# Kernel optimization log

Measured on AMD Instinct MI355X. Metric: run time of the kernel, lower is better.

Reference implementation:

```python
import jax, jax.numpy as jnp
import numpy as np

EMBED_DIM = 1024
NUM_HEADS = 16
HEAD_DIM = EMBED_DIM // NUM_HEADS
SCALING = HEAD_DIM ** -0.5


def setup_inputs() -> dict:
    key = jax.random.key(0)
    ks = jax.random.split(key, 9)
    T, B, E = 2048, 4, EMBED_DIM
    s = 0.02
    return {
        "query": jax.random.normal(ks[0], (T, B, E), dtype=jnp.float32),
        "Wq": jax.random.normal(ks[1], (E, E), dtype=jnp.float32) * s,
        "bq": jnp.zeros((E,), dtype=jnp.float32),
        "Wk": jax.random.normal(ks[2], (E, E), dtype=jnp.float32) * s,
        "bk": jnp.zeros((E,), dtype=jnp.float32),
        "Wv": jax.random.normal(ks[3], (E, E), dtype=jnp.float32) * s,
        "bv": jnp.zeros((E,), dtype=jnp.float32),
        "Wo": jax.random.normal(ks[4], (E, E), dtype=jnp.float32) * s,
        "bo": jnp.zeros((E,), dtype=jnp.float32),
    }


def reference(query, Wq, bq, Wk, bk, Wv, bv, Wo, bo):
    # query: [T, B, E]; torch Linear: x @ W.T + b
    T, B, E = query.shape
    H, D = NUM_HEADS, HEAD_DIM
    q = (query @ Wq.T + bq) * SCALING
    k = query @ Wk.T + bk
    v = query @ Wv.T + bv
    # [T, B, E] -> [B*H, T, D]
    def split_heads(x):
        return x.reshape(T, B * H, D).transpose(1, 0, 2)
    q, k, v = split_heads(q), split_heads(k), split_heads(v)
    attn_weights = jnp.einsum("btd,bsd->bts", q, k)  # [B*H, T, T]
    attn_probs = jax.nn.softmax(attn_weights, axis=-1)
    attn = jnp.einsum("bts,bsd->btd", attn_probs, v)  # [B*H, T, D]
    attn = attn.transpose(1, 0, 2).reshape(T, B, E)
    return attn @ Wo.T + bo
```

## Files before the change

### kernel.cpp

```cpp
#include <hip/hip_runtime.h>
#include <stdint.h>

#define TSEQ   2048
#define BATCH  4
#define NHEAD  16
#define HDIM   64
#define EMB    1024
#define MROWS  (TSEQ * BATCH)
#define QKV_N  (3 * EMB)
#define SCALE_Q 0.125f
#define LOG2E  1.4426950408889634f
#define CB2    (3.0f * LOG2E)

typedef __bf16  bf16x8  __attribute__((ext_vector_type(8)));
typedef __bf16  bf16x2  __attribute__((ext_vector_type(2)));
typedef short   s16x8   __attribute__((ext_vector_type(8)));
typedef float   f32x4   __attribute__((ext_vector_type(4)));
typedef float   f32x16  __attribute__((ext_vector_type(16)));

__device__ __forceinline__ uint16_t b16c(float f) {
    __bf16 h = (__bf16)f;
    return __builtin_bit_cast(uint16_t, h);
}
__device__ __forceinline__ uint32_t pk2(float a, float b) {
    bf16x2 h; h[0] = (__bf16)a; h[1] = (__bf16)b;
    return __builtin_bit_cast(uint32_t, h);
}
__device__ __forceinline__ float exp2hw(float x) {
    float r; asm("v_exp_f32 %0, %1" : "=v"(r) : "v"(x)); return r;
}
__device__ __forceinline__ bf16x8 ldfrag(const uint16_t* p) {
    return __builtin_bit_cast(bf16x8, *(const s16x8*)p);
}
__device__ __forceinline__ f32x4 MFMA(bf16x8 a, bf16x8 b, f32x4 c) {
    return __builtin_amdgcn_mfma_f32_16x16x32_bf16(a, b, c, 0, 0, 0);
}
__device__ __forceinline__ f32x16 MFMA32(bf16x8 a, bf16x8 b, f32x16 c) {
    return __builtin_amdgcn_mfma_f32_32x32x16_bf16(a, b, c, 0, 0, 0);
}

#define GLOAD_LDS16(g, l) \
    __builtin_amdgcn_global_load_lds((const __attribute__((address_space(1))) void*)(g), \
                                     (__attribute__((address_space(3))) void*)(l), 16, 0, 0)

__global__ void cvt_f2b4(const float* __restrict__ src, uint16_t* __restrict__ dst, int n4) {
    int i = blockIdx.x * blockDim.x + threadIdx.x;
    if (i >= n4) return;
    float4 v = ((const float4*)src)[i];
    ushort4 o;
    o.x = b16c(v.x); o.y = b16c(v.y); o.z = b16c(v.z); o.w = b16c(v.w);
    ((ushort4*)dst)[i] = o;
}

__global__ void cvt_wqkv(const float* __restrict__ Wq, const float* __restrict__ Wk,
                         const float* __restrict__ Wv, const float* __restrict__ bq,
                         const float* __restrict__ bk, const float* __restrict__ bv,
                         uint16_t* __restrict__ Wqkv, float* __restrict__ bqkv, int n4) {
    int i = blockIdx.x * blockDim.x + threadIdx.x;
    if (i < QKV_N) {
        float bval;
        if (i < EMB)            bval = bq[i] * SCALE_Q;
        else if (i < 2 * EMB)   bval = bk[i - EMB];
        else                    bval = bv[i - 2 * EMB];
        bqkv[i] = bval;
    }
    if (i >= n4) return;
    int e = i * 4;
    int n = e >> 10;
    int k = e & 1023;
    const float* src; float sc;
    if (n < EMB)            { src = Wq + ((size_t)n << 10) + k;             sc = SCALE_Q; }
    else if (n < 2 * EMB)   { src = Wk + ((size_t)(n - EMB) << 10) + k;     sc = 1.f; }
    else                    { src = Wv + ((size_t)(n - 2 * EMB) << 10) + k; sc = 1.f; }
    float4 v = *(const float4*)src;
    ushort4 o;
    o.x = b16c(v.x * sc); o.y = b16c(v.y * sc); o.z = b16c(v.z * sc); o.w = b16c(v.w * sc);
    ((ushort4*)Wqkv)[i] = o;
}

template <typename CT>
__global__ __launch_bounds__(256) void gemm_bt(
        const uint16_t* __restrict__ A, const uint16_t* __restrict__ Bt,
        const float* __restrict__ bias, CT* __restrict__ C,
        int M, int N, int K, int tiles_n) {
    __shared__ uint16_t As[128 * 32];
    __shared__ uint16_t Bs[128 * 32];

    const int nwg = gridDim.x;
    const int bid0 = blockIdx.x;
    const int bid = (bid0 & 7) * (nwg >> 3) + (bid0 >> 3);
    const int tm = bid / tiles_n, tn = bid % tiles_n;
    const int tid = threadIdx.x;
    const int l = tid & 63, w = tid >> 6;
    const int wm = w >> 1, wn = w & 1;
    const int fr = l & 15, fq = l >> 4;

    f32x4 acc[4][4] = {};

    const int row_a = tid >> 2;
    const int kblk  = (tid & 3) << 3;
    const uint16_t* gA0 = A  + (size_t)(tm * 128 + row_a) * K + kblk;
    const uint16_t* gB0 = Bt + (size_t)(tn * 128 + row_a) * K + kblk;
    const uint16_t* gA1 = gA0 + (size_t)64 * K;
    const uint16_t* gB1 = gB0 + (size_t)64 * K;
    uint16_t* lA0 = As + w * 512;
    uint16_t* lA1 = As + 2048 + w * 512;
    uint16_t* lB0 = Bs + w * 512;
    uint16_t* lB1 = Bs + 2048 + w * 512;

    for (int k0 = 0; k0 < K; k0 += 32) {
        GLOAD_LDS16(gA0 + k0, lA0);
        GLOAD_LDS16(gA1 + k0, lA1);
        GLOAD_LDS16(gB0 + k0, lB0);
        GLOAD_LDS16(gB1 + k0, lB1);
        __syncthreads();

        bf16x8 a[4], b[4];
#pragma unroll
        for (int i = 0; i < 4; i++)
            a[i] = ldfrag(&As[(wm * 64 + i * 16 + fr) * 32 + fq * 8]);
#pragma unroll
        for (int i = 0; i < 4; i++)
            b[i] = ldfrag(&Bs[(wn * 64 + i * 16 + fr) * 32 + fq * 8]);
#pragma unroll
        for (int i = 0; i < 4; i++)
#pragma unroll
            for (int j = 0; j < 4; j++)
                acc[i][j] = MFMA(a[i], b[j], acc[i][j]);
        __syncthreads();
    }

#pragma unroll
    for (int j = 0; j < 4; j++) {
        const int col = tn * 128 + wn * 64 + j * 16 + fr;
        const float bv = bias[col];
#pragma unroll
        for (int i = 0; i < 4; i++) {
#pragma unroll
            for (int r = 0; r < 4; r++) {
                const int row = tm * 128 + wm * 64 + i * 16 + fq * 4 + r;
                const float v = acc[i][j][r] + bv;
                if constexpr (sizeof(CT) == 2) C[(size_t)row * N + col] = (CT)b16c(v);
                else                           C[(size_t)row * N + col] = (CT)v;
            }
        }
    }
}

#define SWZK(r) ((((r) & 3) ^ (((r) >> 2) & 3)))

__global__ __launch_bounds__(512, 2) void gemm_qkv(
        const uint16_t* __restrict__ A, const uint16_t* __restrict__ Bt,
        const float* __restrict__ bias, uint16_t* __restrict__ C) {
    __shared__ __align__(16) uint16_t lds[4 * 16384];

    const int bid0 = blockIdx.x;
    const int bid = (bid0 & 7) * 48 + (bid0 >> 3);
    const int tm = bid / 12, tn = bid % 12;
    const int tid = threadIdx.x;
    const int w = tid >> 6, l = tid & 63;
    const int wm = w >> 2, wn = w & 3;
    const int l5 = l & 31, hi = l >> 5;

    const uint16_t* gA[2]; const uint16_t* gB[2];
    int ldsA[2], ldsB[2];
#pragma unroll
    for (int i = 0; i < 2; i++) {
        int c = i * 512 + tid;
        int row = c >> 2, fqp = c & 3;
        gA[i] = A  + (size_t)(tm * 256 + row) * 1024 + ((fqp ^ SWZK(row)) * 8);
        gB[i] = Bt + (size_t)(tn * 256 + row) * 1024 + ((fqp ^ SWZK(row)) * 8);
        ldsA[i] = (i * 512 + w * 64) * 8;
        ldsB[i] = 8192 + (i * 512 + w * 64) * 8;
    }

    int aoff[4][2], boff[2][2];
#pragma unroll
    for (int mf = 0; mf < 4; mf++) {
        int row = wm * 128 + mf * 32 + l5;
#pragma unroll
        for (int ks = 0; ks < 2; ks++)
            aoff[mf][ks] = row * 32 + (((ks * 2 + hi) ^ SWZK(row)) * 8);
    }
#pragma unroll
    for (int nf = 0; nf < 2; nf++) {
        int row = wn * 64 + nf * 32 + l5;
#pragma unroll
        for (int ks = 0; ks < 2; ks++)
            boff[nf][ks] = 8192 + row * 32 + (((ks * 2 + hi) ^ SWZK(row)) * 8);
    }

    f32x16 acc[4][2] = {};

#define STAGE_T(t, s)                                            \
    {                                                            \
        uint16_t* base_ = lds + (s) * 16384;                     \
        GLOAD_LDS16(gA[0] + (t) * 32, base_ + ldsA[0]);          \
        GLOAD_LDS16(gB[0] + (t) * 32, base_ + ldsB[0]);          \
        GLOAD_LDS16(gA[1] + (t) * 32, base_ + ldsA[1]);          \
        GLOAD_LDS16(gB[1] + (t) * 32, base_ + ldsB[1]);          \
    }

    STAGE_T(0, 0); STAGE_T(1, 1); STAGE_T(2, 2);
    asm volatile("s_waitcnt vmcnt(8)" ::: "memory");
    __builtin_amdgcn_s_barrier();
    __builtin_amdgcn_sched_barrier(0);

    for (int j = 0; j < 32; j++) {
        const int s = j & 3;
        if (j + 3 < 32) STAGE_T(j + 3, (j + 3) & 3);
        const uint16_t* sl = lds + s * 16384;

#pragma unroll
        for (int ks = 0; ks < 2; ks++) {
            bf16x8 af[4], bfg[2];
#pragma unroll
            for (int mf = 0; mf < 4; mf++) af[mf] = ldfrag(sl + aoff[mf][ks]);
#pragma unroll
            for (int nf = 0; nf < 2; nf++) bfg[nf] = ldfrag(sl + boff[nf][ks]);
            __builtin_amdgcn_s_setprio(1);
#pragma unroll
            for (int mf = 0; mf < 4; mf++)
#pragma unroll
                for (int nf = 0; nf < 2; nf++)
                    acc[mf][nf] = MFMA32(af[mf], bfg[nf], acc[mf][nf]);
            __builtin_amdgcn_s_setprio(0);
        }

        __builtin_amdgcn_sched_barrier(0);
        if (j < 29)       asm volatile("s_waitcnt vmcnt(8)" ::: "memory");
        else if (j == 29) asm volatile("s_waitcnt vmcnt(4)" ::: "memory");
        else              asm volatile("s_waitcnt vmcnt(0)" ::: "memory");
        __builtin_amdgcn_s_barrier();
        __builtin_amdgcn_sched_barrier(0);
    }

#pragma unroll
    for (int nf = 0; nf < 2; nf++) {
        const int col = tn * 256 + wn * 64 + nf * 32 + l5;
        const float bv = bias[col];
#pragma unroll
        for (int mf = 0; mf < 4; mf++) {
#pragma unroll
            for (int r = 0; r < 16; r++) {
                const int row = tm * 256 + wm * 128 + mf * 32 + (r & 3) + 8 * (r >> 2) + 4 * hi;
                C[(size_t)row * 3072 + col] = b16c(acc[mf][nf][r] + bv);
            }
        }
    }
#undef STAGE_T
}

__device__ __forceinline__ int swze(int row, int colE) {
    return (row << 6) + (colE ^ ((((row & 7) ^ ((row >> 3) & 7)) & 7) << 3));
}

__device__ __forceinline__ void sm_pv_half(
        f32x16& s0, f32x16& s1, float& lrun,
        const bf16x8 (&vf0)[4], const bf16x8 (&vf1)[4],
        f32x16& oa, f32x16& ob) {
    float rs = 0.f;
#pragma unroll
    for (int kt = 0; kt < 4; kt++) {
        const f32x16& sv = (kt < 2) ? s0 : s1;
        const int base = (kt & 1) * 8;
        float p[8];
#pragma unroll
        for (int i = 0; i < 8; i++)
            p[i] = exp2hw(__builtin_fmaf(sv[base + i], LOG2E, -CB2));
        float r0 = p[0] + p[1], r1 = p[2] + p[3];
        float r2 = p[4] + p[5], r3 = p[6] + p[7];
        rs += (r0 + r1) + (r2 + r3);
        uint32_t k0 = pk2(p[0], p[1]), k1 = pk2(p[2], p[3]);
        uint32_t k2 = pk2(p[4], p[5]), k3 = pk2(p[6], p[7]);
        auto r02 = __builtin_amdgcn_permlane32_swap((int)k0, (int)k2, false, false);
        auto r13 = __builtin_amdgcn_permlane32_swap((int)k1, (int)k3, false, false);
        union { uint32_t u[4]; bf16x8 v; } cv;
        cv.u[0] = (uint32_t)r02[0]; cv.u[1] = (uint32_t)r13[0];
        cv.u[2] = (uint32_t)r02[1]; cv.u[3] = (uint32_t)r13[1];
        oa = MFMA32(vf0[kt], cv.v, oa);
        ob = MFMA32(vf1[kt], cv.v, ob);
    }
    auto rr = __builtin_amdgcn_permlane32_swap(__float_as_int(rs), __float_as_int(rs), false, false);
    lrun += __int_as_float(rr[0]) + __int_as_float(rr[1]);
}

__global__ __launch_bounds__(256, 2) void flash_attn5(
        const uint16_t* __restrict__ qkv, uint16_t* __restrict__ attnb) {
    __shared__ __align__(16) uint16_t smem[16384];
    uint16_t* k0p = smem;
    uint16_t* k1p = smem + 4096;
    uint16_t* v0p = smem + 8192;
    uint16_t* v1p = smem + 12288;

    int bid = (int)blockIdx.x;
    bid = (bid & 7) * 64 + (bid >> 3);
    const int head = bid >> 3;
    const int qt   = bid & 7;
    const int b    = head >> 4, h = head & 15;
    const int tid  = threadIdx.x;
    const int l  = tid & 63, w = tid >> 6;
    const int q5 = l & 31;
    const int hi = l >> 5;
    const size_t tstep = (size_t)64 * 4 * 3072;

    const int qrowA = qt * 256 + w * 64 + q5;
    const uint16_t* qbA = qkv + ((size_t)(qrowA * 4 + b)) * 3072 + h * 64 + hi * 8;
    const uint16_t* qbB = qbA + (size_t)32 * 4 * 3072;
    bf16x8 qA[4], qB[4];
#pragma unroll
    for (int s = 0; s < 4; s++) { qA[s] = ldfrag(qbA + 16 * s); qB[s] = ldfrag(qbB + 16 * s); }

    const int r0 = w * 16 + (l >> 3);
    const int r1 = r0 + 8;
    const int cu0 = (((l & 7) ^ ((r0 & 7) ^ ((r0 >> 3) & 7))) & 7) << 3;
    const int cu1 = (((l & 7) ^ ((r1 & 7) ^ ((r1 >> 3) & 7))) & 7) << 3;
    const uint16_t* gk0 = qkv + ((size_t)(r0 * 4 + b)) * 3072 + 1024 + h * 64 + cu0;
    const uint16_t* gk1 = qkv + ((size_t)(r1 * 4 + b)) * 3072 + 1024 + h * 64 + cu1;
    const int kdst0 = w * 1024;
    const int kdst1 = w * 1024 + 512;

    const int skv  = (tid >> 3) * 2;
    const int scol = (tid & 7) * 8;
    const uint16_t* gv = qkv + ((size_t)(skv * 4 + b)) * 3072 + 2048 + h * 64 + scol;
    int voff[8];
#pragma unroll
    for (int j2 = 0; j2 < 8; j2++)
        voff[j2] = (scol + j2) * 64 + (skv ^ ((((j2 ^ (scol >> 3)) & 7)) << 3));

    GLOAD_LDS16(gk0, k0p + kdst0);
    GLOAD_LDS16(gk1, k0p + kdst1);
    {
        uint4 a0 = *(const uint4*)gv;
        uint4 a1 = *(const uint4*)(gv + 12288);
        const uint16_t* e0 = (const uint16_t*)&a0;
        const uint16_t* e1 = (const uint16_t*)&a1;
#pragma unroll
        for (int j2 = 0; j2 < 8; j2++)
            *(uint32_t*)&v0p[voff[j2]] = (uint32_t)e0[j2] | ((uint32_t)e1[j2] << 16);
    }
    gk0 += tstep; gk1 += tstep; gv += tstep;
    __syncthreads();

    f32x16 o0 = {}, o1 = {}, o2 = {}, o3 = {};
    float lrunA = 0.f, lrunB = 0.f;

    for (int t = 0; t < 32; t++) {
        const uint16_t* kb = (t & 1) ? k1p : k0p;
        const uint16_t* vb = (t & 1) ? v1p : v0p;
        uint16_t* kn = (t & 1) ? k0p : k1p;
        uint16_t* vn = (t & 1) ? v0p : v1p;

        uint4 a0, a1;
        if (t < 31) {
            GLOAD_LDS16(gk0, kn + kdst0);
            GLOAD_LDS16(gk1, kn + kdst1);
            a0 = *(const uint4*)gv;
            a1 = *(const uint4*)(gv + 12288);
            gk0 += tstep; gk1 += tstep; gv += tstep;
        }

        f32x16 sA0 = {}, sA1 = {}, sB0 = {}, sB1 = {};
#pragma unroll
        for (int s = 0; s < 4; s++) {
            bf16x8 kf0 = ldfrag(&kb[swze(q5,      16 * s + 8 * hi)]);
            bf16x8 kf1 = ldfrag(&kb[swze(32 + q5, 16 * s + 8 * hi)]);
            sA0 = MFMA32(kf0, qA[s], sA0);
            sA1 = MFMA32(kf1, qA[s], sA1);
            sB0 = MFMA32(kf0, qB[s], sB0);
            sB1 = MFMA32(kf1, qB[s], sB1);
        }

        bf16x8 vf0[4], vf1[4];
#pragma unroll
        for (int kt = 0; kt < 4; kt++) {
            vf0[kt] = ldfrag(&vb[swze(q5,      16 * kt + 8 * hi)]);
            vf1[kt] = ldfrag(&vb[swze(32 + q5, 16 * kt + 8 * hi)]);
        }

        sm_pv_half(sA0, sA1, lrunA, vf0, vf1, o0, o1);
        sm_pv_half(sB0, sB1, lrunB, vf0, vf1, o2, o3);

        if (t < 31) {
            const uint16_t* e0 = (const uint16_t*)&a0;
            const uint16_t* e1 = (const uint16_t*)&a1;
#pragma unroll
            for (int j2 = 0; j2 < 8; j2++)
                *(uint32_t*)&vn[voff[j2]] = (uint32_t)e0[j2] | ((uint32_t)e1[j2] << 16);
        }
        __syncthreads();
    }

    uint16_t* OstA = smem + w * 4096;
    uint16_t* OstB = OstA + 2048;
#pragma unroll
    for (int half = 0; half < 2; half++) {
        uint16_t* Ost = half ? OstB : OstA;
        const float inv = 1.f / (half ? lrunB : lrunA);
#pragma unroll
        for (int dt = 0; dt < 2; dt++) {
            const f32x16& ov = half ? (dt ? o3 : o2) : (dt ? o1 : o0);
#pragma unroll
            for (int a = 0; a < 4; a++) {
#pragma unroll
                for (int cp = 0; cp < 2; cp++) {
                    const int r = a * 4 + cp * 2;
                    uint32_t dw = pk2(ov[r] * inv, ov[r + 1] * inv);
                    const int d0 = dt * 32 + a * 8 + hi * 4 + cp * 2;
                    *(uint32_t*)&Ost[swze(q5, d0)] = dw;
                }
            }
        }
    }
    const int rq = l >> 1;
#pragma unroll
    for (int half = 0; half < 2; half++) {
        uint16_t* Ost = half ? OstB : OstA;
        const int qrow2 = qt * 256 + w * 64 + half * 32 + rq;
        uint16_t* ob = attnb + ((size_t)(qrow2 * 4 + b)) * 1024 + h * 64;
#pragma unroll
        for (int i = 0; i < 4; i++) {
            const int c4 = (l & 1) * 4 + i;
            uint4 vv = *(const uint4*)&Ost[swze(rq, c4 * 8)];
            *(uint4*)(ob + c4 * 8) = vv;
        }
    }
}

extern "C" void kernel_launch(void* const* d_in, const int* in_sizes, int n_in,
                              void* d_out, int out_size, void* d_ws, size_t ws_size,
                              hipStream_t stream) {
    const float* X  = (const float*)d_in[0];
    const float* Wq = (const float*)d_in[1];
    const float* bq = (const float*)d_in[2];
    const float* Wk = (const float*)d_in[3];
    const float* bk = (const float*)d_in[4];
    const float* Wv = (const float*)d_in[5];
    const float* bv = (const float*)d_in[6];
    const float* Wo = (const float*)d_in[7];
    const float* bo = (const float*)d_in[8];
    float* out = (float*)d_out;

    uint8_t* ws = (uint8_t*)d_ws;
    uint16_t* Xbf   = (uint16_t*)(ws);
    uint16_t* Wqkv  = (uint16_t*)(ws + 16777216);
    uint16_t* Wobf  = (uint16_t*)(ws + 23068672);
    float*    bqkv  = (float*)   (ws + 25165824);
    uint16_t* qkv   = (uint16_t*)(ws + 25178112);
    uint16_t* attnb = (uint16_t*)(ws + 75509760);

    cvt_f2b4<<<(MROWS * EMB / 4 + 255) / 256, 256, 0, stream>>>(X, Xbf, MROWS * EMB / 4);
    cvt_f2b4<<<(EMB * EMB / 4 + 255) / 256, 256, 0, stream>>>(Wo, Wobf, EMB * EMB / 4);
    cvt_wqkv<<<(QKV_N * EMB / 4 + 255) / 256, 256, 0, stream>>>(
        Wq, Wk, Wv, bq, bk, bv, Wqkv, bqkv, QKV_N * EMB / 4);

    gemm_qkv<<<384, 512, 0, stream>>>(Xbf, Wqkv, bqkv, qkv);

    flash_attn5<<<512, 256, 0, stream>>>(qkv, attnb);

    gemm_bt<float><<<(MROWS / 128) * (EMB / 128), 256, 0, stream>>>(
        attnb, Wobf, bo, out, MROWS, EMB, EMB, EMB / 128);
}
```

Measured before the change: 207.9 us.

## Unify QKV and output projections into triple-buffered 256x128 GEMM kernel

```diff
diff --git a/kernel.cpp b/kernel.cpp
--- a/kernel.cpp
+++ b/kernel.cpp
@@ -31,9 +31,6 @@
 }
 __device__ __forceinline__ bf16x8 ldfrag(const uint16_t* p) {
     return __builtin_bit_cast(bf16x8, *(const s16x8*)p);
-}
-__device__ __forceinline__ f32x4 MFMA(bf16x8 a, bf16x8 b, f32x4 c) {
-    return __builtin_amdgcn_mfma_f32_16x16x32_bf16(a, b, c, 0, 0, 0);
 }
 __device__ __forceinline__ f32x16 MFMA32(bf16x8 a, bf16x8 b, f32x16 c) {
     return __builtin_amdgcn_mfma_f32_32x32x16_bf16(a, b, c, 0, 0, 0);
@@ -78,177 +75,114 @@
     ((ushort4*)Wqkv)[i] = o;
 }
 
-template <typename CT>
-__global__ __launch_bounds__(256) void gemm_bt(
+template <int TILES_N, typename CT>
+__global__ __launch_bounds__(512, 1) void gemm_3buf(
         const uint16_t* __restrict__ A, const uint16_t* __restrict__ Bt,
-        const float* __restrict__ bias, CT* __restrict__ C,
-        int M, int N, int K, int tiles_n) {
-    __shared__ uint16_t As[128 * 32];
-    __shared__ uint16_t Bs[128 * 32];
-
-    const int nwg = gridDim.x;
+        const float* __restrict__ bias, CT* __restrict__ C) {
+    __shared__ __align__(16) uint16_t lds[3 * 24576];
+
+    const int nwg = 32 * TILES_N;
     const int bid0 = blockIdx.x;
     const int bid = (bid0 & 7) * (nwg >> 3) + (bid0 >> 3);
-    const int tm = bid / tiles_n, tn = bid % tiles_n;
+    const int tm = bid / TILES_N, tn = bid % TILES_N;
     const int tid = threadIdx.x;
-    const int l = tid & 63, w = tid >> 6;
+    const int w = tid >> 6, l = tid & 63;
     const int wm = w >> 1, wn = w & 1;
-    const int fr = l & 15, fq = l >> 4;
-
-    f32x4 acc[4][4] = {};
-
-    const int row_a = tid >> 2;
-    const int kblk  = (tid & 3) << 3;
-    const uint16_t* gA0 = A  + (size_t)(tm * 128 + row_a) * K + kblk;
-    const uint16_t* gB0 = Bt + (size_t)(tn * 128 + row_a) * K + kblk;
-    const uint16_t* gA1 = gA0 + (size_t)64 * K;
-    const uint16_t* gB1 = gB0 + (size_t)64 * K;
-    uint16_t* lA0 = As + w * 512;
-    uint16_t* lA1 = As + 2048 + w * 512;
-    uint16_t* lB0 = Bs + w * 512;
-    uint16_t* lB1 = Bs + 2048 + w * 512;
-
-    for (int k0 = 0; k0 < K; k0 += 32) {
-        GLOAD_LDS16(gA0 + k0, lA0);
-        GLOAD_LDS16(gA1 + k0, lA1);
-        GLOAD_LDS16(gB0 + k0, lB0);
-        GLOAD_LDS16(gB1 + k0, lB1);
-        __syncthreads();
-
-        bf16x8 a[4], b[4];
-#pragma unroll
-        for (int i = 0; i < 4; i++)
-            a[i] = ldfrag(&As[(wm * 64 + i * 16 + fr) * 32 + fq * 8]);
-#pragma unroll
-        for (int i = 0; i < 4; i++)
-            b[i] = ldfrag(&Bs[(wn * 64 + i * 16 + fr) * 32 + fq * 8]);
-#pragma unroll
-        for (int i = 0; i < 4; i++)
-#pragma unroll
-            for (int j = 0; j < 4; j++)
-                acc[i][j] = MFMA(a[i], b[j], acc[i][j]);
-        __syncthreads();
-    }
-
-#pragma unroll
-    for (int j = 0; j < 4; j++) {
-        const int col = tn * 128 + wn * 64 + j * 16 + fr;
+    const int l5 = l & 31, hi = l >> 5;
+    const int N = TILES_N * 128;
+    (void)w;
+
+    const uint16_t* gsrc[6];
+    int ldst[6];
+#pragma unroll
+    for (int i = 0; i < 6; i++) {
+        int p = i * 512 + tid;
+        if (p < 2048) {
+            int r = p >> 3, cp = p & 7;
+            gsrc[i] = A + (size_t)(tm * 256 + r) * 1024 + ((cp ^ (r & 7)) * 8);
+            ldst[i] = p * 8;
+        } else {
+            int q = p - 2048;
+            int r = q >> 3, cp = q & 7;
+            gsrc[i] = Bt + (size_t)(tn * 128 + r) * 1024 + ((cp ^ (r & 7)) * 8);
+            ldst[i] = 16384 + q * 8;
+        }
+    }
+
+    int aoff[2][4], boff[2][4];
+#pragma unroll
+    for (int mf = 0; mf < 2; mf++) {
+        int r = wm * 64 + mf * 32 + l5;
+#pragma unroll
+        for (int ks = 0; ks < 4; ks++)
+            aoff[mf][ks] = r * 64 + (((ks * 2 + hi) ^ (r & 7)) * 8);
+    }
+#pragma unroll
+    for (int nf = 0; nf < 2; nf++) {
+        int r = wn * 64 + nf * 32 + l5;
+#pragma unroll
+        for (int ks = 0; ks < 4; ks++)
+            boff[nf][ks] = 16384 + r * 64 + (((ks * 2 + hi) ^ (r & 7)) * 8);
+    }
+
+    f32x16 acc[2][2] = {};
+
+#define STAGE3(t, s)                                         \
+    {                                                        \
+        uint16_t* bb = lds + (s) * 24576;                    \
+        GLOAD_LDS16(gsrc[0] + (t) * 64, bb + ldst[0]);       \
+        GLOAD_LDS16(gsrc[1] + (t) * 64, bb + ldst[1]);       \
+        GLOAD_LDS16(gsrc[2] + (t) * 64, bb + ldst[2]);       \
+        GLOAD_LDS16(gsrc[3] + (t) * 64, bb + ldst[3]);       \
+        GLOAD_LDS16(gsrc[4] + (t) * 64, bb + ldst[4]);       \
+        GLOAD_LDS16(gsrc[5] + (t) * 64, bb + ldst[5]);       \
+    }
+
+    STAGE3(0, 0);
+    STAGE3(1, 1);
+    asm volatile("s_waitcnt vmcnt(6)" ::: "memory");
+    __builtin_amdgcn_s_barrier();
+
+#pragma unroll
+    for (int t = 0; t < 16; t++) {
+        const uint16_t* sl = lds + (t % 3) * 24576;
+        if (t + 2 < 16) STAGE3(t + 2, (t + 2) % 3);
+
+#pragma unroll
+        for (int ks = 0; ks < 4; ks++) {
+            bf16x8 af0 = ldfrag(sl + aoff[0][ks]);
+            bf16x8 af1 = ldfrag(sl + aoff[1][ks]);
+            bf16x8 bf0 = ldfrag(sl + boff[0][ks]);
+            bf16x8 bf1 = ldfrag(sl + boff[1][ks]);
+            __builtin_amdgcn_s_setprio(1);
+            acc[0][0] = MFMA32(af0, bf0, acc[0][0]);
+            acc[0][1] = MFMA32(af0, bf1, acc[0][1]);
+            acc[1][0] = MFMA32(af1, bf0, acc[1][0]);
+            acc[1][1] = MFMA32(af1, bf1, acc[1][1]);
+            __builtin_amdgcn_s_setprio(0);
+        }
+
+        if (t < 14)       asm volatile("s_waitcnt vmcnt(6)" ::: "memory");
+        else if (t == 14) asm volatile("s_waitcnt vmcnt(0)" ::: "memory");
+        __builtin_amdgcn_s_barrier();
+    }
+#undef STAGE3
+
+#pragma unroll
+    for (int nf = 0; nf < 2; nf++) {
+        const int col = tn * 128 + wn * 64 + nf * 32 + l5;
         const float bv = bias[col];
 #pragma unroll
-        for (int i = 0; i < 4; i++) {
-#pragma unroll
-            for (int r = 0; r < 4; r++) {
-                const int row = tm * 128 + wm * 64 + i * 16 + fq * 4 + r;
-                const float v = acc[i][j][r] + bv;
+        for (int mf = 0; mf < 2; mf++) {
+#pragma unroll
+            for (int r = 0; r < 16; r++) {
+                const int row = tm * 256 + wm * 64 + mf * 32 + (r & 3) + 8 * (r >> 2) + 4 * hi;
+                const float v = acc[mf][nf][r] + bv;
                 if constexpr (sizeof(CT) == 2) C[(size_t)row * N + col] = (CT)b16c(v);
                 else                           C[(size_t)row * N + col] = (CT)v;
             }
         }
     }
-}
-
-#define SWZK(r) ((((r) & 3) ^ (((r) >> 2) & 3)))
-
-__global__ __launch_bounds__(512, 2) void gemm_qkv(
-        const uint16_t* __restrict__ A, const uint16_t* __restrict__ Bt,
-        const float* __restrict__ bias, uint16_t* __restrict__ C) {
-    __shared__ __align__(16) uint16_t lds[4 * 16384];
-
-    const int bid0 = blockIdx.x;
-    const int bid = (bid0 & 7) * 48 + (bid0 >> 3);
-    const int tm = bid / 12, tn = bid % 12;
-    const int tid = threadIdx.x;
-    const int w = tid >> 6, l = tid & 63;
-    const int wm = w >> 2, wn = w & 3;
-    const int l5 = l & 31, hi = l >> 5;
-
-    const uint16_t* gA[2]; const uint16_t* gB[2];
-    int ldsA[2], ldsB[2];
-#pragma unroll
-    for (int i = 0; i < 2; i++) {
-        int c = i * 512 + tid;
-        int row = c >> 2, fqp = c & 3;
-        gA[i] = A  + (size_t)(tm * 256 + row) * 1024 + ((fqp ^ SWZK(row)) * 8);
-        gB[i] = Bt + (size_t)(tn * 256 + row) * 1024 + ((fqp ^ SWZK(row)) * 8);
-        ldsA[i] = (i * 512 + w * 64) * 8;
-        ldsB[i] = 8192 + (i * 512 + w * 64) * 8;
-    }
-
-    int aoff[4][2], boff[2][2];
-#pragma unroll
-    for (int mf = 0; mf < 4; mf++) {
-        int row = wm * 128 + mf * 32 + l5;
-#pragma unroll
-        for (int ks = 0; ks < 2; ks++)
-            aoff[mf][ks] = row * 32 + (((ks * 2 + hi) ^ SWZK(row)) * 8);
-    }
-#pragma unroll
-    for (int nf = 0; nf < 2; nf++) {
-        int row = wn * 64 + nf * 32 + l5;
-#pragma unroll
-        for (int ks = 0; ks < 2; ks++)
-            boff[nf][ks] = 8192 + row * 32 + (((ks * 2 + hi) ^ SWZK(row)) * 8);
-    }
-
-    f32x16 acc[4][2] = {};
-
-#define STAGE_T(t, s)                                            \
-    {                                                            \
-        uint16_t* base_ = lds + (s) * 16384;                     \
-        GLOAD_LDS16(gA[0] + (t) * 32, base_ + ldsA[0]);          \
-        GLOAD_LDS16(gB[0] + (t) * 32, base_ + ldsB[0]);          \
-        GLOAD_LDS16(gA[1] + (t) * 32, base_ + ldsA[1]);          \
-        GLOAD_LDS16(gB[1] + (t) * 32, base_ + ldsB[1]);          \
-    }
-
-    STAGE_T(0, 0); STAGE_T(1, 1); STAGE_T(2, 2);
-    asm volatile("s_waitcnt vmcnt(8)" ::: "memory");
-    __builtin_amdgcn_s_barrier();
-    __builtin_amdgcn_sched_barrier(0);
-
-    for (int j = 0; j < 32; j++) {
-        const int s = j & 3;
-        if (j + 3 < 32) STAGE_T(j + 3, (j + 3) & 3);
-        const uint16_t* sl = lds + s * 16384;
-
-#pragma unroll
-        for (int ks = 0; ks < 2; ks++) {
-            bf16x8 af[4], bfg[2];
-#pragma unroll
-            for (int mf = 0; mf < 4; mf++) af[mf] = ldfrag(sl + aoff[mf][ks]);
-#pragma unroll
-            for (int nf = 0; nf < 2; nf++) bfg[nf] = ldfrag(sl + boff[nf][ks]);
-            __builtin_amdgcn_s_setprio(1);
-#pragma unroll
-            for (int mf = 0; mf < 4; mf++)
-#pragma unroll
-                for (int nf = 0; nf < 2; nf++)
-                    acc[mf][nf] = MFMA32(af[mf], bfg[nf], acc[mf][nf]);
-            __builtin_amdgcn_s_setprio(0);
-        }
-
-        __builtin_amdgcn_sched_barrier(0);
-        if (j < 29)       asm volatile("s_waitcnt vmcnt(8)" ::: "memory");
-        else if (j == 29) asm volatile("s_waitcnt vmcnt(4)" ::: "memory");
-        else              asm volatile("s_waitcnt vmcnt(0)" ::: "memory");
-        __builtin_amdgcn_s_barrier();
-        __builtin_amdgcn_sched_barrier(0);
-    }
-
-#pragma unroll
-    for (int nf = 0; nf < 2; nf++) {
-        const int col = tn * 256 + wn * 64 + nf * 32 + l5;
-        const float bv = bias[col];
-#pragma unroll
-        for (int mf = 0; mf < 4; mf++) {
-#pragma unroll
-            for (int r = 0; r < 16; r++) {
-                const int row = tm * 256 + wm * 128 + mf * 32 + (r & 3) + 8 * (r >> 2) + 4 * hi;
-                C[(size_t)row * 3072 + col] = b16c(acc[mf][nf][r] + bv);
-            }
-        }
-    }
-#undef STAGE_T
 }
 
 __device__ __forceinline__ int swze(int row, int colE) {
@@ -454,10 +388,9 @@
     cvt_wqkv<<<(QKV_N * EMB / 4 + 255) / 256, 256, 0, stream>>>(
         Wq, Wk, Wv, bq, bk, bv, Wqkv, bqkv, QKV_N * EMB / 4);
 
-    gemm_qkv<<<384, 512, 0, stream>>>(Xbf, Wqkv, bqkv, qkv);
+    gemm_3buf<24, uint16_t><<<768, 512, 0, stream>>>(Xbf, Wqkv, bqkv, qkv);
 
     flash_attn5<<<512, 256, 0, stream>>>(qkv, attnb);
 
-    gemm_bt<float><<<(MROWS / 128) * (EMB / 128), 256, 0, stream>>>(
-        attnb, Wobf, bo, out, MROWS, EMB, EMB, EMB / 128);
-}
+    gemm_3buf<8, float><<<256, 512, 0, stream>>>(attnb, Wobf, bo, out);
+}
```

Result: faster. 202.6 us (-2.6%).
